# Performance work log

Hardware: AMD Instinct MI355X
Metric: run time of the kernel (lower is better)

Reference implementation:

```python
import jax, jax.numpy as jnp
import numpy as np
from jax.ops import segment_sum, segment_max

N_GENE, D_IN, HID, HEADS = 100000, 128, 128, 4
N_DRUG, N_DIS = 10000, 5000


def gcn_conv(x, src, dst, W, b, n):
    # PyG GCNConv: add self loops, symmetric deg^-1/2 normalization, scatter-add
    h = x @ W  # [n, hid]
    loop = jnp.arange(n)
    s = jnp.concatenate([src, loop])
    d = jnp.concatenate([dst, loop])
    deg = segment_sum(jnp.ones(d.shape[0], h.dtype), d, num_segments=n)
    dis = jnp.where(deg > 0, jax.lax.rsqrt(deg), 0.0)
    norm = dis[s] * dis[d]  # [E+n]
    return segment_sum(h[s] * norm[:, None], d, num_segments=n) + b


def gat_conv(xs, xd, src, dst, W, att_s, att_d, b, n_dst, heads=HEADS):
    # PyG GATConv (bipartite, shared lin, add_self_loops=False, concat=False)
    C = W.shape[1] // heads
    hs = (xs @ W).reshape(-1, heads, C)  # [Ns,H,C]
    hd = (xd @ W).reshape(-1, heads, C)  # [Nd,H,C]
    a_s = (hs * att_s).sum(-1)  # [Ns,H]
    a_d = (hd * att_d).sum(-1)  # [Nd,H]
    e = jax.nn.leaky_relu(a_s[src] + a_d[dst], 0.2)  # [E,H]
    m = segment_max(e, dst, num_segments=n_dst)
    m = jnp.where(jnp.isfinite(m), m, 0.0)
    ex = jnp.exp(e - m[dst])
    denom = segment_sum(ex, dst, num_segments=n_dst)
    alpha = ex / (denom[dst] + 1e-16)  # per-dst softmax
    out = segment_sum(hs[src] * alpha[:, :, None], dst, num_segments=n_dst)  # [Nd,H,C]
    return out.mean(axis=1) + b


def setup_inputs() -> dict:
    key = jax.random.key(0)
    ks = jax.random.split(key, 24)
    Eg, Ed, Ec = 1000000, 250000, 250000
    sc = 1.0 / np.sqrt(HID)
    inp = {
        'gene_nodes': jax.random.normal(ks[0], (N_GENE, D_IN), jnp.float32),
        'drug_edges': jnp.stack([jax.random.randint(ks[1], (Ed,), 0, N_DRUG),
                                 jax.random.randint(ks[2], (Ed,), 0, N_GENE)]),
        'disease_edges': jnp.stack([jax.random.randint(ks[3], (Ec,), 0, N_DIS),
                                    jax.random.randint(ks[4], (Ec,), 0, N_GENE)]),
        'gene_edges': jax.random.randint(ks[5], (2, Eg), 0, N_GENE),
        'gcn1_w': jax.random.normal(ks[6], (D_IN, HID), jnp.float32) * sc,
        'gcn1_b': jnp.zeros((HID,), jnp.float32),
        'gcn2_w': jax.random.normal(ks[7], (HID, HID), jnp.float32) * sc,
        'gcn2_b': jnp.zeros((HID,), jnp.float32),
        'drug_embed': jax.random.normal(ks[8], (N_DRUG, HID), jnp.float32),
        'disease_embed': jax.random.normal(ks[9], (N_DIS, HID), jnp.float32),
        'gat_d_w': jax.random.normal(ks[10], (HID, HEADS * HID), jnp.float32) * sc,
        'gat_d_att_src': jax.random.normal(ks[11], (HEADS, HID), jnp.float32) * sc,
        'gat_d_att_dst': jax.random.normal(ks[12], (HEADS, HID), jnp.float32) * sc,
        'gat_d_b': jnp.zeros((HID,), jnp.float32),
        'gat_c_w': jax.random.normal(ks[13], (HID, HEADS * HID), jnp.float32) * sc,
        'gat_c_att_src': jax.random.normal(ks[14], (HEADS, HID), jnp.float32) * sc,
        'gat_c_att_dst': jax.random.normal(ks[15], (HEADS, HID), jnp.float32) * sc,
        'gat_c_b': jnp.zeros((HID,), jnp.float32),
        'fuse_w': jax.random.normal(ks[16], (3 * HID, HID), jnp.float32) * sc,
        'fuse_b': jnp.zeros((HID,), jnp.float32),
    }
    return inp


def reference(gene_nodes, drug_edges, disease_edges, gene_edges,
              gcn1_w, gcn1_b, gcn2_w, gcn2_b, drug_embed, disease_embed,
              gat_d_w, gat_d_att_src, gat_d_att_dst, gat_d_b,
              gat_c_w, gat_c_att_src, gat_c_att_dst, gat_c_b,
              fuse_w, fuse_b):
    gs, gd = gene_edges[0], gene_edges[1]
    x = jax.nn.relu(gcn_conv(gene_nodes, gs, gd, gcn1_w, gcn1_b, N_GENE))
    x = jax.nn.relu(gcn_conv(x, gs, gd, gcn2_w, gcn2_b, N_GENE))
    # hetero GAT: drug->gene and disease->gene, HeteroConv aggr='mean'
    g_drug = gat_conv(drug_embed, x, drug_edges[0], drug_edges[1],
                      gat_d_w, gat_d_att_src, gat_d_att_dst, gat_d_b, N_GENE)
    g_dis = gat_conv(disease_embed, x, disease_edges[0], disease_edges[1],
                     gat_c_w, gat_c_att_src, gat_c_att_dst, gat_c_b, N_GENE)
    gene_out = 0.5 * (g_drug + g_dis)
    bg = gene_out.mean(axis=0, keepdims=True)   # [1,HID]
    bd = drug_embed.mean(axis=0, keepdims=True)
    bc = disease_embed.mean(axis=0, keepdims=True)
    return jnp.concatenate([bg, bd, bc], axis=-1) @ fuse_w + fuse_b  # [1,HID]
```

## Files before the change

kernel.cpp:

```cpp
#include <hip/hip_runtime.h>
#include <hip/hip_fp16.h>

#define NG 100000
#define NDR 10000
#define NDI 5000
#define NDOM (3 * NG + NDR + NDI)
#define NBUCK 616
#define BCHUNK 4096
#define EPT 16

typedef _Float16 f16x8 __attribute__((ext_vector_type(8)));
typedef float f32x4 __attribute__((ext_vector_type(4)));

__device__ __forceinline__ void atomAddF(float* p, float v) { unsafeAtomicAdd(p, v); }

static inline int cdiv_h(int a, int b) { return (a + b - 1) / b; }

__device__ __host__ __forceinline__ int bcap(int b) {
  return b < 586 ? 8192 : (b < 606 ? 24576 : 32768);
}
__device__ __host__ __forceinline__ int bbase(int b) {
  if (b < 586) return b * 8192;
  if (b < 606) return 586 * 8192 + (b - 586) * 24576;
  return 586 * 8192 + 20 * 24576 + (b - 606) * 32768;
}
#define NPAIR (586 * 8192 + 20 * 24576 + 10 * 32768)

__global__ __launch_bounds__(256) void k_front(const float* __restrict__ W1,
                                               const float* __restrict__ W2,
                                               const float* __restrict__ Wd,
                                               const float* __restrict__ Wc,
                                               const float* __restrict__ attd_d,
                                               const float* __restrict__ attd_c,
                                               __half* __restrict__ Wt1,
                                               __half* __restrict__ Wt2,
                                               __half* __restrict__ Wtd,
                                               __half* __restrict__ Wtc,
                                               float* __restrict__ watt,
                                               int* __restrict__ cursor616,
                                               const float* __restrict__ xd,
                                               float* __restrict__ od,
                                               const float* __restrict__ xc,
                                               float* __restrict__ oc) {
  int blk = blockIdx.x;
  int t = threadIdx.x;
  if (blk < 40) {
    __shared__ float tile[64][65];
    const float* W;
    __half* Wt;
    int N, k0, n0;
    if (blk < 4) { W = W1; Wt = Wt1; N = 128; k0 = (blk >> 1) * 64; n0 = (blk & 1) * 64; }
    else if (blk < 8) { int b = blk - 4; W = W2; Wt = Wt2; N = 128; k0 = (b >> 1) * 64; n0 = (b & 1) * 64; }
    else if (blk < 24) { int b = blk - 8; W = Wd; Wt = Wtd; N = 512; k0 = (b >> 3) * 64; n0 = (b & 7) * 64; }
    else { int b = blk - 24; W = Wc; Wt = Wtc; N = 512; k0 = (b >> 3) * 64; n0 = (b & 7) * 64; }
    for (int i = t; i < 4096; i += 256) {
      int r = i >> 6, c = i & 63;
      tile[r][c] = W[(size_t)(k0 + r) * N + n0 + c];
    }
    __syncthreads();
    for (int i = t; i < 4096; i += 256) {
      int k = i & 63, n = i >> 6;
      Wt[(size_t)(n0 + n) * 128 + k0 + k] = __float2half(tile[k][n]);
    }
    return;
  }
  if (blk < 44) {
    int slot = (blk - 40) * 256 + t;
    int i = slot >> 3, s8 = slot & 7;
    const float* W = (s8 < 4) ? Wd : Wc;
    const float* A = (s8 < 4) ? attd_d : attd_c;
    int h = s8 & 3;
    float s = 0.f;
    for (int cc = 0; cc < 128; cc++) s += W[(size_t)i * 512 + h * 128 + cc] * A[h * 128 + cc];
    watt[i * 8 + s8] = s;
    return;
  }
  if (blk == 44) {
    for (int i = t; i < NBUCK; i += 256) cursor616[i] = bbase(i);
    return;
  }
  int cb = blk - 45;
  int q = cb >= 79;
  const float* x = q ? xc : xd;
  float* o = q ? oc : od;
  int N = q ? NDI : NDR;
  int r0 = (q ? cb - 79 : cb) * 128 + (t >> 7) * 64;
  int col = t & 127;
  int r1 = min(r0 + 64, N);
  float acc = 0.f;
  for (int r = r0; r < r1; r++) acc += x[(size_t)r * 128 + col];
  if (r0 < N) atomAddF(&o[col], acc);
}

__device__ __forceinline__ void decode(int idx, const int* __restrict__ ge, int Eg_,
                                       const int* __restrict__ de, int Ed_,
                                       const int* __restrict__ ce, int Ec_,
                                       unsigned& node, unsigned& val) {
  int B1 = Eg_, B2 = Eg_ + Ed_, B3 = Eg_ + 2 * Ed_, B4 = B3 + Ec_;
  if (idx < B1) { node = (unsigned)ge[Eg_ + idx]; val = (unsigned)ge[idx]; }
  else if (idx < B2) { int i = idx - B1; node = NG + (unsigned)de[Ed_ + i]; val = (unsigned)de[i]; }
  else if (idx < B3) { int i = idx - B2; node = 3 * NG + (unsigned)de[i]; val = (unsigned)de[Ed_ + i]; }
  else if (idx < B4) { int i = idx - B3; node = 2 * NG + (unsigned)ce[Ec_ + i]; val = (unsigned)ce[i]; }
  else { int i = idx - B4; node = 3 * NG + NDR + (unsigned)ce[i]; val = (unsigned)ce[Ec_ + i]; }
}

__global__ __launch_bounds__(256) void k_binH(const int* __restrict__ ge, int Eg_,
                                              const int* __restrict__ de, int Ed_,
                                              const int* __restrict__ ce, int Ec_,
                                              int* __restrict__ cursor616,
                                              unsigned* __restrict__ pairs) {
  __shared__ int hist[NBUCK];
  int t = threadIdx.x;
  for (int i = t; i < NBUCK; i += 256) hist[i] = 0;
  __syncthreads();
  const int ME = Eg_ + 2 * (Ed_ + Ec_);
  int base = blockIdx.x * BCHUNK;
  int cnt = min(BCHUNK, ME - base);

  unsigned nodeR[EPT], valR[EPT];
#pragma unroll
  for (int k = 0; k < EPT; k++) {
    int j = t + k * 256;
    nodeR[k] = 0xFFFFFFFFu;
    if (j < cnt) decode(base + j, ge, Eg_, de, Ed_, ce, Ec_, nodeR[k], valR[k]);
  }
#pragma unroll
  for (int k = 0; k < EPT; k++)
    if (nodeR[k] != 0xFFFFFFFFu) atomicAdd(&hist[nodeR[k] >> 9], 1);
  __syncthreads();
  for (int b = t; b < NBUCK; b += 256) {
    int h = hist[b];
    hist[b] = h ? atomicAdd(&cursor616[b], h) : 0;
  }
  __syncthreads();
#pragma unroll
  for (int k = 0; k < EPT; k++) {
    if (nodeR[k] == 0xFFFFFFFFu) continue;
    unsigned b = nodeR[k] >> 9;
    int p = atomicAdd(&hist[b], 1);
    if (p < bbase(b) + bcap(b))
      pairs[p] = ((nodeR[k] - (b << 9)) << 17) | valR[k];
  }
}

__global__ __launch_bounds__(256) void k_scan616(const int* __restrict__ cursor616,
                                                 int* __restrict__ bucketbase) {
  __shared__ int s[256];
  int t = threadIdx.x;
  int loc[3];
  int sum = 0;
#pragma unroll
  for (int k = 0; k < 3; k++) {
    int b = 3 * t + k;
    int v = (b < NBUCK) ? min(cursor616[b] - bbase(b), bcap(b)) : 0;
    loc[k] = sum;
    sum += v;
  }
  s[t] = sum;
  __syncthreads();
  for (int off = 1; off < 256; off <<= 1) {
    int add = (t >= off) ? s[t - off] : 0;
    __syncthreads();
    s[t] += add;
    __syncthreads();
  }
  int excl = s[t] - sum;
#pragma unroll
  for (int k = 0; k < 3; k++) {
    int b = 3 * t + k;
    if (b < NBUCK) bucketbase[b] = excl + loc[k];
  }
}

__global__ __launch_bounds__(256) void k_placeAll(const int* __restrict__ cursor616,
                                                  const int* __restrict__ bucketbase,
                                                  const unsigned* __restrict__ pairs,
                                                  int* __restrict__ rowptr,
                                                  float* __restrict__ dis,
                                                  int* __restrict__ adj) {
  __shared__ int hist[512];
  __shared__ int scan[256];
  int b = blockIdx.x;
  int n0 = b << 9;
  int n1 = min(n0 + 512, NDOM);
  int t = threadIdx.x;
  hist[t] = 0;
  hist[t + 256] = 0;
  __syncthreads();
  int base = bbase(b);
  int cnt = min(cursor616[b] - base, bcap(b));
  for (int i = base + t; i < base + cnt; i += 256) atomicAdd(&hist[pairs[i] >> 17], 1);
  __syncthreads();
  int h0 = hist[2 * t], h1 = hist[2 * t + 1];
  int sum = h0 + h1;
  scan[t] = sum;
  __syncthreads();
  for (int off = 1; off < 256; off <<= 1) {
    int add = (t >= off) ? scan[t - off] : 0;
    __syncthreads();
    scan[t] += add;
    __syncthreads();
  }
  int excl = scan[t] - sum;
  int bb = bucketbase[b];
  int i0 = 2 * t, i1 = 2 * t + 1;
  int r0 = bb + excl, r1 = bb + excl + h0;
  if (n0 + i0 < n1) {
    rowptr[n0 + i0] = r0;
    if (n0 + i0 < NG) dis[n0 + i0] = rsqrtf((float)h0 + 1.0f);
  }
  if (n0 + i1 < n1) {
    rowptr[n0 + i1] = r1;
    if (n0 + i1 < NG) dis[n0 + i1] = rsqrtf((float)h1 + 1.0f);
    if (n0 + i1 == NDOM - 1) rowptr[NDOM] = r1 + h1;
  }
  if (n0 + i0 == NDOM - 1) rowptr[NDOM] = r0 + h0;
  __syncthreads();
  hist[i0] = r0;
  hist[i1] = r1;
  __syncthreads();
  for (int i = base + t; i < base + cnt; i += 256) {
    unsigned pr = pairs[i];
    int p = atomicAdd(&hist[pr >> 17], 1);
    adj[p] = (int)(pr & 0x1FFFFu);
  }
}

template <int INF16>
__device__ __forceinline__ void mgemm_body(char* lds, int bx, const void* __restrict__ Xv,
                                           const __half* __restrict__ Wt, int M,
                                           const float* __restrict__ dis,
                                           __half* __restrict__ hh) {
  char* As = lds;
  char* Bs = lds + 16 * 1024;
  const int t = threadIdx.x;
  const int row0 = bx * 64;

#pragma unroll
  for (int rep = 0; rep < 8; rep++) {
    int q = t + rep * 256;
    int r = q >> 4, c16 = (q & 15) * 16;
    uint4 v = *(const uint4*)((const char*)Wt + r * 256 + c16);
    *(uint4*)(Bs + ((r * 256 + c16) ^ ((r & 7) << 4))) = v;
  }
  if (INF16 == 0) {
    const float* X = (const float*)Xv;
#pragma unroll
    for (int rep = 0; rep < 8; rep++) {
      int q = t + rep * 256;
      int r = q >> 5, c4 = (q & 31) * 4;
      int gr = row0 + r;
      float4 xv = make_float4(0.f, 0.f, 0.f, 0.f);
      if (gr < M) xv = *(const float4*)&X[(size_t)gr * 128 + c4];
      __half2 h0 = __floats2half2_rn(xv.x, xv.y);
      __half2 h1 = __floats2half2_rn(xv.z, xv.w);
      uint2 pk;
      pk.x = *(unsigned*)&h0;
      pk.y = *(unsigned*)&h1;
      *(uint2*)(As + ((r * 256 + c4 * 2) ^ ((r & 7) << 4))) = pk;
    }
  } else {
    const __half* X = (const __half*)Xv;
#pragma unroll
    for (int rep = 0; rep < 4; rep++) {
      int q = t + rep * 256;
      int r = q >> 4, c16 = (q & 15) * 16;
      int gr = row0 + r;
      uint4 v = make_uint4(0u, 0u, 0u, 0u);
      if (gr < M) v = *(const uint4*)((const char*)X + (size_t)gr * 256 + c16);
      *(uint4*)(As + ((r * 256 + c16) ^ ((r & 7) << 4))) = v;
    }
  }
  __syncthreads();

  const int w = t >> 6, l = t & 63;
  const int lr = l & 15, lk = l >> 4;
  f32x4 acc[8] = {};
#pragma unroll
  for (int s = 0; s < 4; s++) {
    int arow = w * 16 + lr;
    f16x8 a = *(const f16x8*)(As + ((arow * 256 + lk * 16 + s * 64) ^ ((arow & 7) << 4)));
#pragma unroll
    for (int nt = 0; nt < 8; nt++) {
      int brow = nt * 16 + lr;
      f16x8 b = *(const f16x8*)(Bs + ((brow * 256 + lk * 16 + s * 64) ^ ((brow & 7) << 4)));
      acc[nt] = __builtin_amdgcn_mfma_f32_16x16x32_f16(a, b, acc[nt], 0, 0, 0);
    }
  }
  float ddv[4];
  int rowb = row0 + w * 16 + lk * 4;
#pragma unroll
  for (int j = 0; j < 4; j++) ddv[j] = (rowb + j < M) ? dis[rowb + j] : 0.f;
#pragma unroll
  for (int nt = 0; nt < 8; nt++) {
#pragma unroll
    for (int j = 0; j < 4; j++) {
      int row = rowb + j;
      if (row < M) hh[(size_t)row * 128 + nt * 16 + lr] = __float2half(acc[nt][j] * ddv[j]);
    }
  }
}

__device__ __forceinline__ void mgat_body(char* lds, int bxx, int h,
                                          const float* __restrict__ Xd,
                                          const float* __restrict__ Xc,
                                          const __half* __restrict__ Wtd,
                                          const __half* __restrict__ Wtc,
                                          const float* __restrict__ attSd,
                                          const float* __restrict__ attSc,
                                          __half* __restrict__ hsd,
                                          __half* __restrict__ hsc,
                                          float* __restrict__ a_s_d,
                                          float* __restrict__ a_s_c) {
  char* As = lds;
  char* Bs = lds + 16 * 1024;
  const int t = threadIdx.x;
  const int nbd = (NDR + 63) >> 6;
  const int q = bxx >= nbd;
  const int bx = q ? bxx - nbd : bxx;
  const int M = q ? NDI : NDR;
  const float* X = q ? Xc : Xd;
  const __half* Wt = q ? Wtc : Wtd;
  const float* attS = q ? attSc : attSd;
  __half* hs = q ? hsc : hsd;
  float* a_s = q ? a_s_c : a_s_d;
  const int row0 = bx * 64;
  const __half* Wth = Wt + (size_t)h * 128 * 128;

#pragma unroll
  for (int rep = 0; rep < 8; rep++) {
    int r = (t + rep * 256) >> 4, c16 = ((t + rep * 256) & 15) * 16;
    uint4 v = *(const uint4*)((const char*)Wth + r * 256 + c16);
    *(uint4*)(Bs + ((r * 256 + c16) ^ ((r & 7) << 4))) = v;
  }
#pragma unroll
  for (int rep = 0; rep < 8; rep++) {
    int qq = t + rep * 256;
    int r = qq >> 5, c4 = (qq & 31) * 4;
    int gr = row0 + r;
    float4 xv = make_float4(0.f, 0.f, 0.f, 0.f);
    if (gr < M) xv = *(const float4*)&X[(size_t)gr * 128 + c4];
    __half2 h0 = __floats2half2_rn(xv.x, xv.y);
    __half2 h1 = __floats2half2_rn(xv.z, xv.w);
    uint2 pk;
    pk.x = *(unsigned*)&h0;
    pk.y = *(unsigned*)&h1;
    *(uint2*)(As + ((r * 256 + c4 * 2) ^ ((r & 7) << 4))) = pk;
  }
  __syncthreads();

  const int w = t >> 6, l = t & 63;
  const int lr = l & 15, lk = l >> 4;
  f32x4 acc[8] = {};
#pragma unroll
  for (int s = 0; s < 4; s++) {
    int arow = w * 16 + lr;
    f16x8 a = *(const f16x8*)(As + ((arow * 256 + lk * 16 + s * 64) ^ ((arow & 7) << 4)));
#pragma unroll
    for (int nt = 0; nt < 8; nt++) {
      int brow = nt * 16 + lr;
      f16x8 b = *(const f16x8*)(Bs + ((brow * 256 + lk * 16 + s * 64) ^ ((brow & 7) << 4)));
      acc[nt] = __builtin_amdgcn_mfma_f32_16x16x32_f16(a, b, acc[nt], 0, 0, 0);
    }
  }
  float av[8];
#pragma unroll
  for (int nt = 0; nt < 8; nt++) av[nt] = attS[h * 128 + nt * 16 + lr];

  int rowb = row0 + w * 16 + lk * 4;
  float p[4] = {0.f, 0.f, 0.f, 0.f};
#pragma unroll
  for (int nt = 0; nt < 8; nt++) {
#pragma unroll
    for (int j = 0; j < 4; j++) {
      int row = rowb + j;
      if (row < M) hs[(size_t)row * 512 + h * 128 + nt * 16 + lr] = __float2half(acc[nt][j]);
      p[j] += acc[nt][j] * av[nt];
    }
  }
#pragma unroll
  for (int m = 1; m < 16; m <<= 1) {
#pragma unroll
    for (int j = 0; j < 4; j++) p[j] += __shfl_xor(p[j], m);
  }
  if (lr == 0) {
#pragma unroll
    for (int j = 0; j < 4; j++) {
      int row = rowb + j;
      if (row < M) a_s[(size_t)row * 4 + h] = p[j];
    }
  }
}

__global__ __launch_bounds__(256) void k_mm1(const float* __restrict__ X1,
                                             const __half* __restrict__ Wt1,
                                             const float* __restrict__ dis,
                                             __half* __restrict__ hh,
                                             const float* __restrict__ Xd,
                                             const float* __restrict__ Xc,
                                             const __half* __restrict__ Wtd,
                                             const __half* __restrict__ Wtc,
                                             const float* __restrict__ attSd,
                                             const float* __restrict__ attSc,
                                             __half* __restrict__ hsd,
                                             __half* __restrict__ hsc,
                                             float* __restrict__ a_s_d,
                                             float* __restrict__ a_s_c) {
  __shared__ __align__(16) char lds[48 * 1024];
  const int NB1 = (NG + 63) >> 6;
  if ((int)blockIdx.x < NB1) {
    mgemm_body<0>(lds, blockIdx.x, X1, Wt1, NG, dis, hh);
    return;
  }
  int r = blockIdx.x - NB1;
  mgat_body(lds, r >> 2, r & 3, Xd, Xc, Wtd, Wtc, attSd, attSc, hsd, hsc, a_s_d, a_s_c);
}

template <int INF16>
__global__ __launch_bounds__(256) void k_mgemm(const void* __restrict__ Xv,
                                               const __half* __restrict__ Wt, int M,
                                               const float* __restrict__ dis,
                                               __half* __restrict__ hh) {
  __shared__ __align__(16) char lds[48 * 1024];
  mgemm_body<INF16>(lds, blockIdx.x, Xv, Wt, M, dis, hh);
}

template <int FIN>
__global__ __launch_bounds__(256) void k_gather(const __half* __restrict__ hh,
                                                const int* __restrict__ rowptr,
                                                const int* __restrict__ adj,
                                                const float* __restrict__ dis,
                                                const float* __restrict__ b,
                                                const float* __restrict__ watt,
                                                void* __restrict__ outv, int n) {
  int wid = threadIdx.x >> 6;
  int lane = threadIdx.x & 63;
  int d = blockIdx.x * 4 + wid;
  if (d >= n) return;
  int p0 = rowptr[d], p1 = rowptr[d + 1];
  int c = lane * 2;
  float2 s;
  {
    unsigned v = *(const unsigned*)&hh[(size_t)d * 128 + c];
    s = __half22float2(*(__half2*)&v);
  }
  for (int base = p0; base < p1; base += 64) {
    int remain = p1 - base;
    int m = remain < 64 ? remain : 64;
    int idx = (lane < m) ? adj[base + lane] : 0;
    int j = 0;
    for (; j + 8 <= m; j += 8) {
      int nb[8];
      unsigned v[8];
#pragma unroll
      for (int u = 0; u < 8; u++) nb[u] = __shfl(idx, j + u);
#pragma unroll
      for (int u = 0; u < 8; u++) v[u] = *(const unsigned*)&hh[(size_t)nb[u] * 128 + c];
#pragma unroll
      for (int u = 0; u < 8; u++) {
        float2 f = __half22float2(*(__half2*)&v[u]);
        s.x += f.x;
        s.y += f.y;
      }
    }
    for (; j + 4 <= m; j += 4) {
      int nb[4];
      unsigned v[4];
#pragma unroll
      for (int u = 0; u < 4; u++) nb[u] = __shfl(idx, j + u);
#pragma unroll
      for (int u = 0; u < 4; u++) v[u] = *(const unsigned*)&hh[(size_t)nb[u] * 128 + c];
#pragma unroll
      for (int u = 0; u < 4; u++) {
        float2 f = __half22float2(*(__half2*)&v[u]);
        s.x += f.x;
        s.y += f.y;
      }
    }
    for (; j < m; j++) {
      int nb = __shfl(idx, j);
      unsigned v = *(const unsigned*)&hh[(size_t)nb * 128 + c];
      float2 f = __half22float2(*(__half2*)&v);
      s.x += f.x;
      s.y += f.y;
    }
  }
  float dd = dis[d];
  float x0 = fmaxf(dd * s.x + b[c], 0.f);
  float x1v = fmaxf(dd * s.y + b[c + 1], 0.f);
  if (FIN == 1) {
    __half* o = (__half*)outv;
    __half2 hv = __floats2half2_rn(x0, x1v);
    *(__half2*)&o[(size_t)d * 128 + c] = hv;
  } else {
    float* o = (float*)outv;
    float p[8];
    const float* w0 = &watt[c * 8];
#pragma unroll
    for (int h = 0; h < 8; h++) p[h] = x0 * w0[h] + x1v * w0[8 + h];
#pragma unroll
    for (int mm = 32; mm; mm >>= 1) {
#pragma unroll
      for (int h = 0; h < 8; h++) p[h] += __shfl_xor(p[h], mm);
    }
    if (lane == 0) {
      *(float4*)&o[(size_t)d * 8] = make_float4(p[0], p[1], p[2], p[3]);
      *(float4*)&o[(size_t)d * 8 + 4] = make_float4(p[4], p[5], p[6], p[7]);
    }
  }
}

__global__ __launch_bounds__(256) void k_edgeA(const int* __restrict__ rowptr,
                                               const int* __restrict__ adj,
                                               const float* __restrict__ a_s_d,
                                               const float* __restrict__ a_s_c,
                                               const float* __restrict__ att,
                                               float* __restrict__ denom_d,
                                               float* __restrict__ denom_c) {
  int nb1 = (NG + 255) >> 8;
  int blk = blockIdx.x;
  int q = blk >= nb1;
  int d = (blk - (q ? nb1 : 0)) * 256 + threadIdx.x;
  if (d >= NG) return;
  const int* rp = rowptr + NG + (q ? NG : 0);
  const float* a_s = q ? a_s_c : a_s_d;
  float* den = q ? denom_c : denom_d;
  int p0 = rp[d], p1 = rp[d + 1];
  float4 ad4 = *(const float4*)&att[(size_t)d * 8 + q * 4];
  float4 acc = make_float4(0.f, 0.f, 0.f, 0.f);
  for (int p = p0; p < p1; p++) {
    int s = adj[p];
    float4 as4 = *(const float4*)&a_s[(size_t)s * 4];
    float v0 = as4.x + ad4.x, v1 = as4.y + ad4.y, v2 = as4.z + ad4.z, v3 = as4.w + ad4.w;
    v0 = v0 > 0.f ? v0 : 0.2f * v0;
    v1 = v1 > 0.f ? v1 : 0.2f * v1;
    v2 = v2 > 0.f ? v2 : 0.2f * v2;
    v3 = v3 > 0.f ? v3 : 0.2f * v3;
    acc.x += __expf(fminf(v0, 50.f));
    acc.y += __expf(fminf(v1, 50.f));
    acc.z += __expf(fminf(v2, 50.f));
    acc.w += __expf(fminf(v3, 50.f));
  }
  *(float4*)&den[(size_t)d * 4] = acc;
}

__global__ __launch_bounds__(256) void k_edgeB(const int* __restrict__ rowptr,
                                               const int* __restrict__ adj,
                                               const float* __restrict__ a_s_d,
                                               const float* __restrict__ a_s_c,
                                               const float* __restrict__ att,
                                               const float* __restrict__ denom_d,
                                               const float* __restrict__ denom_c,
                                               float* __restrict__ wsrc_d,
                                               float* __restrict__ wsrc_c) {
  int gw = (blockIdx.x * 256 + threadIdx.x) >> 6;
  int lane = threadIdx.x & 63;
  int q = gw >= NDR;
  int s = q ? gw - NDR : gw;
  if (q && s >= NDI) return;
  const int* rp = rowptr + 3 * NG + (q ? NDR : 0);
  const float* a_s = q ? a_s_c : a_s_d;
  const float* den = q ? denom_c : denom_d;
  float* ws = q ? wsrc_c : wsrc_d;
  int p0 = rp[s], p1 = rp[s + 1];
  float4 as4 = *(const float4*)&a_s[(size_t)s * 4];
  int attoff = q * 4;
  float4 acc = make_float4(0.f, 0.f, 0.f, 0.f);
  for (int p = p0 + lane; p < p1; p += 64) {
    int d = adj[p];
    float4 ad4 = *(const float4*)&att[(size_t)d * 8 + attoff];
    float4 dn = *(const float4*)&den[(size_t)d * 4];
    float v0 = as4.x + ad4.x, v1 = as4.y + ad4.y, v2 = as4.z + ad4.z, v3 = as4.w + ad4.w;
    v0 = v0 > 0.f ? v0 : 0.2f * v0;
    v1 = v1 > 0.f ? v1 : 0.2f * v1;
    v2 = v2 > 0.f ? v2 : 0.2f * v2;
    v3 = v3 > 0.f ? v3 : 0.2f * v3;
    acc.x += __expf(fminf(v0, 50.f)) / (dn.x + 1e-16f);
    acc.y += __expf(fminf(v1, 50.f)) / (dn.y + 1e-16f);
    acc.z += __expf(fminf(v2, 50.f)) / (dn.z + 1e-16f);
    acc.w += __expf(fminf(v3, 50.f)) / (dn.w + 1e-16f);
  }
#pragma unroll
  for (int m = 1; m < 64; m <<= 1) {
    acc.x += __shfl_xor(acc.x, m);
    acc.y += __shfl_xor(acc.y, m);
    acc.z += __shfl_xor(acc.z, m);
    acc.w += __shfl_xor(acc.w, m);
  }
  if (lane == 0) *(float4*)&ws[(size_t)s * 4] = acc;
}

__global__ __launch_bounds__(512) void k_sum(const __half* __restrict__ hs_d,
                                             const float* __restrict__ wsrc_d,
                                             float* __restrict__ S_d,
                                             const __half* __restrict__ hs_c,
                                             const float* __restrict__ wsrc_c,
                                             float* __restrict__ S_c) {
  int t = threadIdx.x;
  const int nws_d = (NDR + 63) >> 6;
  int blk = blockIdx.x;
  int q = blk >= nws_d;
  const __half* hs = q ? hs_c : hs_d;
  const float* wsrc = q ? wsrc_c : wsrc_d;
  float* S = q ? S_c : S_d;
  int N = q ? NDI : NDR;
  int r0 = (q ? blk - nws_d : blk) * 64;
  int h = t >> 7;
  int r1 = min(r0 + 64, N);
  float acc = 0.f;
  for (int r = r0; r < r1; r++) acc += wsrc[r * 4 + h] * __half2float(hs[(size_t)r * 512 + t]);
  atomAddF(&S[t], acc);
}

__global__ __launch_bounds__(128) void k_final(const float* __restrict__ S_d,
                                               const float* __restrict__ S_c,
                                               const float* __restrict__ bdsum,
                                               const float* __restrict__ bcsum,
                                               const float* __restrict__ bd_bias,
                                               const float* __restrict__ bc_bias,
                                               const float* __restrict__ fuse_w,
                                               const float* __restrict__ fuse_b,
                                               float* __restrict__ out) {
  __shared__ float cat[384];
  int t = threadIdx.x;
  float sd = S_d[t] + S_d[128 + t] + S_d[256 + t] + S_d[384 + t];
  float sc = S_c[t] + S_c[128 + t] + S_c[256 + t] + S_c[384 + t];
  const float inv = 1.0f / (4.0f * (float)NG);
  cat[t] = 0.5f * (sd * inv + bd_bias[t] + sc * inv + bc_bias[t]);
  cat[128 + t] = bdsum[t] * (1.0f / (float)NDR);
  cat[256 + t] = bcsum[t] * (1.0f / (float)NDI);
  __syncthreads();
  float o = fuse_b[t];
  for (int k = 0; k < 384; k++) o += cat[k] * fuse_w[k * 128 + t];
  out[t] = o;
}

extern "C" void kernel_launch(void* const* d_in, const int* in_sizes, int n_in,
                              void* d_out, int out_size, void* d_ws, size_t ws_size,
                              hipStream_t stream) {
  const float* gene_nodes   = (const float*)d_in[0];
  const int*   drug_edges   = (const int*)d_in[1];
  const int*   dise_edges   = (const int*)d_in[2];
  const int*   gene_edges   = (const int*)d_in[3];
  const float* gcn1_w       = (const float*)d_in[4];
  const float* gcn1_b       = (const float*)d_in[5];
  const float* gcn2_w       = (const float*)d_in[6];
  const float* gcn2_b       = (const float*)d_in[7];
  const float* drug_embed   = (const float*)d_in[8];
  const float* dise_embed   = (const float*)d_in[9];
  const float* gat_d_w      = (const float*)d_in[10];
  const float* gat_d_att_s  = (const float*)d_in[11];
  const float* gat_d_att_d  = (const float*)d_in[12];
  const float* gat_d_b      = (const float*)d_in[13];
  const float* gat_c_w      = (const float*)d_in[14];
  const float* gat_c_att_s  = (const float*)d_in[15];
  const float* gat_c_att_d  = (const float*)d_in[16];
  const float* gat_c_b      = (const float*)d_in[17];
  const float* fuse_w       = (const float*)d_in[18];
  const float* fuse_b       = (const float*)d_in[19];
  const int Ed = in_sizes[1] / 2;
  const int Ec = in_sizes[2] / 2;
  const int Eg = in_sizes[3] / 2;
  float* out = (float*)d_out;
  (void)n_in; (void)out_size; (void)ws_size;

  const int ME = Eg + 2 * (Ed + Ec);

  char* w = (char*)d_ws;
  auto alloc = [&](size_t n) {
    char* p = w;
    w += (n + 511) & ~(size_t)511;
    return p;
  };
  char* z0 = w;
  float* S_d        = (float*)alloc(512 * 4);
  float* S_c        = (float*)alloc(512 * 4);
  float* bdsum      = (float*)alloc(512);
  float* bcsum      = (float*)alloc(512);
  size_t zbytes = (size_t)(w - z0);
  float* denom_d    = (float*)alloc((size_t)NG * 16);
  float* denom_c    = (float*)alloc((size_t)NG * 16);
  float* wsrc_d     = (float*)alloc((size_t)NDR * 16);
  float* wsrc_c     = (float*)alloc((size_t)NDI * 16);
  float* dis        = (float*)alloc((size_t)NG * 4);
  float* watt       = (float*)alloc(128 * 8 * 4);
  float* att        = (float*)alloc((size_t)NG * 8 * 4);
  float* a_s_d      = (float*)alloc((size_t)NDR * 16);
  float* a_s_c      = (float*)alloc((size_t)NDI * 16);
  int* rowptr       = (int*)alloc((size_t)(NDOM + 1) * 4);
  int* cursor616    = (int*)alloc((size_t)NBUCK * 4);
  int* bucketbase   = (int*)alloc((size_t)(NBUCK + 1) * 4);
  int* adj          = (int*)alloc((size_t)ME * 4);
  unsigned* pairs   = (unsigned*)alloc((size_t)NPAIR * 4);
  __half* Wt1       = (__half*)alloc((size_t)128 * 128 * 2);
  __half* Wt2       = (__half*)alloc((size_t)128 * 128 * 2);
  __half* Wtd       = (__half*)alloc((size_t)512 * 128 * 2);
  __half* Wtc       = (__half*)alloc((size_t)512 * 128 * 2);
  __half* hh        = (__half*)alloc((size_t)NG * 128 * 2);
  __half* x1        = (__half*)alloc((size_t)NG * 128 * 2);
  __half* hs_d      = (__half*)alloc((size_t)NDR * 512 * 2);
  __half* hs_c      = (__half*)alloc((size_t)NDI * 512 * 2);

  hipMemsetAsync(z0, 0, zbytes, stream);

  k_front<<<164, 256, 0, stream>>>(gcn1_w, gcn2_w, gat_d_w, gat_c_w, gat_d_att_d, gat_c_att_d,
                                   Wt1, Wt2, Wtd, Wtc, watt, cursor616,
                                   drug_embed, bdsum, dise_embed, bcsum);

  k_binH<<<cdiv_h(ME, BCHUNK), 256, 0, stream>>>(gene_edges, Eg, drug_edges, Ed, dise_edges, Ec,
                                                 cursor616, pairs);
  k_scan616<<<1, 256, 0, stream>>>(cursor616, bucketbase);
  k_placeAll<<<NBUCK, 256, 0, stream>>>(cursor616, bucketbase, pairs, rowptr, dis, adj);

  int nb1 = cdiv_h(NG, 64);
  int nbg = (cdiv_h(NDR, 64) + cdiv_h(NDI, 64)) * 4;
  k_mm1<<<nb1 + nbg, 256, 0, stream>>>(gene_nodes, Wt1, dis, hh,
                                       drug_embed, dise_embed, Wtd, Wtc,
                                       gat_d_att_s, gat_c_att_s, hs_d, hs_c, a_s_d, a_s_c);

  k_gather<1><<<cdiv_h(NG, 4), 256, 0, stream>>>(hh, rowptr, adj, dis, gcn1_b, nullptr, x1, NG);

  k_mgemm<1><<<nb1, 256, 0, stream>>>(x1, Wt2, NG, dis, hh);
  k_gather<2><<<cdiv_h(NG, 4), 256, 0, stream>>>(hh, rowptr, adj, dis, gcn2_b, watt, att, NG);

  k_edgeA<<<2 * cdiv_h(NG, 256), 256, 0, stream>>>(rowptr, adj, a_s_d, a_s_c, att, denom_d, denom_c);
  k_edgeB<<<cdiv_h((NDR + NDI) * 64, 256), 256, 0, stream>>>(rowptr, adj, a_s_d, a_s_c, att,
                                                             denom_d, denom_c, wsrc_d, wsrc_c);

  k_sum<<<cdiv_h(NDR, 64) + cdiv_h(NDI, 64), 512, 0, stream>>>(hs_d, wsrc_d, S_d,
                                                               hs_c, wsrc_c, S_c);

  k_final<<<1, 128, 0, stream>>>(S_d, S_c, bdsum, bcsum, gat_d_b, gat_c_b, fuse_w, fuse_b, out);
}
```

Baseline: 328.3 us.

## Store GCN features in FP8 and merge edge binning into front kernel

The per-node GCN intermediate features written by the GEMMs and read by the neighbor gather are now stored as FP8 instead of FP16. This halves the bytes moved in the random-access gather over a million edges. Separately, the edge-binning pass is merged into the weight-transpose/front kernel, with zero-initialized counts replacing the precomputed cursor, which removes one launch and one dependency. FP8 storage adds quantization error to the GCN activations and may break accuracy tolerance.

```diff
diff --git a/kernel.cpp b/kernel.cpp
--- a/kernel.cpp
+++ b/kernel.cpp
@@ -11,8 +11,17 @@
 
 typedef _Float16 f16x8 __attribute__((ext_vector_type(8)));
 typedef float f32x4 __attribute__((ext_vector_type(4)));
+typedef float f32x2 __attribute__((ext_vector_type(2)));
 
 __device__ __forceinline__ void atomAddF(float* p, float v) { unsafeAtomicAdd(p, v); }
+
+__device__ __forceinline__ float2 fp8x2_f32(unsigned short v) {
+  f32x2 r = __builtin_amdgcn_cvt_pk_f32_fp8((int)v, false);
+  return make_float2(r[0], r[1]);
+}
+__device__ __forceinline__ unsigned char f32_fp8(float v) {
+  return (unsigned char)(__builtin_amdgcn_cvt_pk_fp8_f32(v, v, 0, false) & 0xFF);
+}
 
 static inline int cdiv_h(int a, int b) { return (a + b - 1) / b; }
 
@@ -26,7 +35,24 @@
 }
 #define NPAIR (586 * 8192 + 20 * 24576 + 10 * 32768)
 
-__global__ __launch_bounds__(256) void k_front(const float* __restrict__ W1,
+__device__ __forceinline__ void decode(int idx, const int* __restrict__ ge, int Eg_,
+                                       const int* __restrict__ de, int Ed_,
+                                       const int* __restrict__ ce, int Ec_,
+                                       unsigned& node, unsigned& val) {
+  int B1 = Eg_, B2 = Eg_ + Ed_, B3 = Eg_ + 2 * Ed_, B4 = B3 + Ec_;
+  if (idx < B1) { node = (unsigned)ge[Eg_ + idx]; val = (unsigned)ge[idx]; }
+  else if (idx < B2) { int i = idx - B1; node = NG + (unsigned)de[Ed_ + i]; val = (unsigned)de[i]; }
+  else if (idx < B3) { int i = idx - B2; node = 3 * NG + (unsigned)de[i]; val = (unsigned)de[Ed_ + i]; }
+  else if (idx < B4) { int i = idx - B3; node = 2 * NG + (unsigned)ce[Ec_ + i]; val = (unsigned)ce[i]; }
+  else { int i = idx - B4; node = 3 * NG + NDR + (unsigned)ce[i]; val = (unsigned)ce[Ec_ + i]; }
+}
+
+__global__ __launch_bounds__(256) void k_build(const int* __restrict__ ge, int Eg_,
+                                               const int* __restrict__ de, int Ed_,
+                                               const int* __restrict__ ce, int Ec_,
+                                               int* __restrict__ count616,
+                                               unsigned* __restrict__ pairs,
+                                               const float* __restrict__ W1,
                                                const float* __restrict__ W2,
                                                const float* __restrict__ Wd,
                                                const float* __restrict__ Wc,
@@ -37,22 +63,56 @@
                                                __half* __restrict__ Wtd,
                                                __half* __restrict__ Wtc,
                                                float* __restrict__ watt,
-                                               int* __restrict__ cursor616,
                                                const float* __restrict__ xd,
                                                float* __restrict__ od,
                                                const float* __restrict__ xc,
                                                float* __restrict__ oc) {
+  const int ME = Eg_ + 2 * (Ed_ + Ec_);
+  const int NBB = (ME + BCHUNK - 1) / BCHUNK;
   int blk = blockIdx.x;
   int t = threadIdx.x;
-  if (blk < 40) {
+  if (blk < NBB) {
+    __shared__ int hist[NBUCK];
+    for (int i = t; i < NBUCK; i += 256) hist[i] = 0;
+    __syncthreads();
+    int base = blk * BCHUNK;
+    int cnt = min(BCHUNK, ME - base);
+    unsigned nodeR[EPT], valR[EPT];
+#pragma unroll
+    for (int k = 0; k < EPT; k++) {
+      int j = t + k * 256;
+      nodeR[k] = 0xFFFFFFFFu;
+      if (j < cnt) decode(base + j, ge, Eg_, de, Ed_, ce, Ec_, nodeR[k], valR[k]);
+    }
+#pragma unroll
+    for (int k = 0; k < EPT; k++)
+      if (nodeR[k] != 0xFFFFFFFFu) atomicAdd(&hist[nodeR[k] >> 9], 1);
+    __syncthreads();
+    for (int b = t; b < NBUCK; b += 256) {
+      int h = hist[b];
+      hist[b] = h ? (bbase(b) + atomicAdd(&count616[b], h)) : 0;
+    }
+    __syncthreads();
+#pragma unroll
+    for (int k = 0; k < EPT; k++) {
+      if (nodeR[k] == 0xFFFFFFFFu) continue;
+      unsigned b = nodeR[k] >> 9;
+      int p = atomicAdd(&hist[b], 1);
+      if (p < bbase(b) + bcap(b))
+        pairs[p] = ((nodeR[k] - (b << 9)) << 17) | valR[k];
+    }
+    return;
+  }
+  int fb = blk - NBB;
+  if (fb < 40) {
     __shared__ float tile[64][65];
     const float* W;
     __half* Wt;
     int N, k0, n0;
-    if (blk < 4) { W = W1; Wt = Wt1; N = 128; k0 = (blk >> 1) * 64; n0 = (blk & 1) * 64; }
-    else if (blk < 8) { int b = blk - 4; W = W2; Wt = Wt2; N = 128; k0 = (b >> 1) * 64; n0 = (b & 1) * 64; }
-    else if (blk < 24) { int b = blk - 8; W = Wd; Wt = Wtd; N = 512; k0 = (b >> 3) * 64; n0 = (b & 7) * 64; }
-    else { int b = blk - 24; W = Wc; Wt = Wtc; N = 512; k0 = (b >> 3) * 64; n0 = (b & 7) * 64; }
+    if (fb < 4) { W = W1; Wt = Wt1; N = 128; k0 = (fb >> 1) * 64; n0 = (fb & 1) * 64; }
+    else if (fb < 8) { int b = fb - 4; W = W2; Wt = Wt2; N = 128; k0 = (b >> 1) * 64; n0 = (b & 1) * 64; }
+    else if (fb < 24) { int b = fb - 8; W = Wd; Wt = Wtd; N = 512; k0 = (b >> 3) * 64; n0 = (b & 7) * 64; }
+    else { int b = fb - 24; W = Wc; Wt = Wtc; N = 512; k0 = (b >> 3) * 64; n0 = (b & 7) * 64; }
     for (int i = t; i < 4096; i += 256) {
       int r = i >> 6, c = i & 63;
       tile[r][c] = W[(size_t)(k0 + r) * N + n0 + c];
@@ -64,8 +124,8 @@
     }
     return;
   }
-  if (blk < 44) {
-    int slot = (blk - 40) * 256 + t;
+  if (fb < 44) {
+    int slot = (fb - 40) * 256 + t;
     int i = slot >> 3, s8 = slot & 7;
     const float* W = (s8 < 4) ? Wd : Wc;
     const float* A = (s8 < 4) ? attd_d : attd_c;
@@ -75,11 +135,7 @@
     watt[i * 8 + s8] = s;
     return;
   }
-  if (blk == 44) {
-    for (int i = t; i < NBUCK; i += 256) cursor616[i] = bbase(i);
-    return;
-  }
-  int cb = blk - 45;
+  int cb = fb - 44;
   int q = cb >= 79;
   const float* x = q ? xc : xd;
   float* o = q ? oc : od;
@@ -92,58 +148,7 @@
   if (r0 < N) atomAddF(&o[col], acc);
 }
 
-__device__ __forceinline__ void decode(int idx, const int* __restrict__ ge, int Eg_,
-                                       const int* __restrict__ de, int Ed_,
-                                       const int* __restrict__ ce, int Ec_,
-                                       unsigned& node, unsigned& val) {
-  int B1 = Eg_, B2 = Eg_ + Ed_, B3 = Eg_ + 2 * Ed_, B4 = B3 + Ec_;
-  if (idx < B1) { node = (unsigned)ge[Eg_ + idx]; val = (unsigned)ge[idx]; }
-  else if (idx < B2) { int i = idx - B1; node = NG + (unsigned)de[Ed_ + i]; val = (unsigned)de[i]; }
-  else if (idx < B3) { int i = idx - B2; node = 3 * NG + (unsigned)de[i]; val = (unsigned)de[Ed_ + i]; }
-  else if (idx < B4) { int i = idx - B3; node = 2 * NG + (unsigned)ce[Ec_ + i]; val = (unsigned)ce[i]; }
-  else { int i = idx - B4; node = 3 * NG + NDR + (unsigned)ce[i]; val = (unsigned)ce[Ec_ + i]; }
-}
-
-__global__ __launch_bounds__(256) void k_binH(const int* __restrict__ ge, int Eg_,
-                                              const int* __restrict__ de, int Ed_,
-                                              const int* __restrict__ ce, int Ec_,
-                                              int* __restrict__ cursor616,
-                                              unsigned* __restrict__ pairs) {
-  __shared__ int hist[NBUCK];
-  int t = threadIdx.x;
-  for (int i = t; i < NBUCK; i += 256) hist[i] = 0;
-  __syncthreads();
-  const int ME = Eg_ + 2 * (Ed_ + Ec_);
-  int base = blockIdx.x * BCHUNK;
-  int cnt = min(BCHUNK, ME - base);
-
-  unsigned nodeR[EPT], valR[EPT];
-#pragma unroll
-  for (int k = 0; k < EPT; k++) {
-    int j = t + k * 256;
-    nodeR[k] = 0xFFFFFFFFu;
-    if (j < cnt) decode(base + j, ge, Eg_, de, Ed_, ce, Ec_, nodeR[k], valR[k]);
-  }
-#pragma unroll
-  for (int k = 0; k < EPT; k++)
-    if (nodeR[k] != 0xFFFFFFFFu) atomicAdd(&hist[nodeR[k] >> 9], 1);
-  __syncthreads();
-  for (int b = t; b < NBUCK; b += 256) {
-    int h = hist[b];
-    hist[b] = h ? atomicAdd(&cursor616[b], h) : 0;
-  }
-  __syncthreads();
-#pragma unroll
-  for (int k = 0; k < EPT; k++) {
-    if (nodeR[k] == 0xFFFFFFFFu) continue;
-    unsigned b = nodeR[k] >> 9;
-    int p = atomicAdd(&hist[b], 1);
-    if (p < bbase(b) + bcap(b))
-      pairs[p] = ((nodeR[k] - (b << 9)) << 17) | valR[k];
-  }
-}
-
-__global__ __launch_bounds__(256) void k_scan616(const int* __restrict__ cursor616,
+__global__ __launch_bounds__(256) void k_scan616(const int* __restrict__ count616,
                                                  int* __restrict__ bucketbase) {
   __shared__ int s[256];
   int t = threadIdx.x;
@@ -152,7 +157,7 @@
 #pragma unroll
   for (int k = 0; k < 3; k++) {
     int b = 3 * t + k;
-    int v = (b < NBUCK) ? min(cursor616[b] - bbase(b), bcap(b)) : 0;
+    int v = (b < NBUCK) ? min(count616[b], bcap(b)) : 0;
     loc[k] = sum;
     sum += v;
   }
@@ -172,7 +177,7 @@
   }
 }
 
-__global__ __launch_bounds__(256) void k_placeAll(const int* __restrict__ cursor616,
+__global__ __launch_bounds__(256) void k_placeAll(const int* __restrict__ count616,
                                                   const int* __restrict__ bucketbase,
                                                   const unsigned* __restrict__ pairs,
                                                   int* __restrict__ rowptr,
@@ -188,7 +193,7 @@
   hist[t + 256] = 0;
   __syncthreads();
   int base = bbase(b);
-  int cnt = min(cursor616[b] - base, bcap(b));
+  int cnt = min(count616[b], bcap(b));
   for (int i = base + t; i < base + cnt; i += 256) atomicAdd(&hist[pairs[i] >> 17], 1);
   __syncthreads();
   int h0 = hist[2 * t], h1 = hist[2 * t + 1];
@@ -230,7 +235,7 @@
 __device__ __forceinline__ void mgemm_body(char* lds, int bx, const void* __restrict__ Xv,
                                            const __half* __restrict__ Wt, int M,
                                            const float* __restrict__ dis,
-                                           __half* __restrict__ hh) {
+                                           unsigned char* __restrict__ hh) {
   char* As = lds;
   char* Bs = lds + 16 * 1024;
   const int t = threadIdx.x;
@@ -296,7 +301,7 @@
 #pragma unroll
     for (int j = 0; j < 4; j++) {
       int row = rowb + j;
-      if (row < M) hh[(size_t)row * 128 + nt * 16 + lr] = __float2half(acc[nt][j] * ddv[j]);
+      if (row < M) hh[(size_t)row * 128 + nt * 16 + lr] = f32_fp8(acc[nt][j] * ddv[j]);
     }
   }
 }
@@ -395,7 +400,7 @@
 __global__ __launch_bounds__(256) void k_mm1(const float* __restrict__ X1,
                                              const __half* __restrict__ Wt1,
                                              const float* __restrict__ dis,
-                                             __half* __restrict__ hh,
+                                             unsigned char* __restrict__ hh,
                                              const float* __restrict__ Xd,
                                              const float* __restrict__ Xc,
                                              const __half* __restrict__ Wtd,
@@ -420,13 +425,13 @@
 __global__ __launch_bounds__(256) void k_mgemm(const void* __restrict__ Xv,
                                                const __half* __restrict__ Wt, int M,
                                                const float* __restrict__ dis,
-                                               __half* __restrict__ hh) {
+                                               unsigned char* __restrict__ hh) {
   __shared__ __align__(16) char lds[48 * 1024];
   mgemm_body<INF16>(lds, blockIdx.x, Xv, Wt, M, dis, hh);
 }
 
 template <int FIN>
-__global__ __launch_bounds__(256) void k_gather(const __half* __restrict__ hh,
+__global__ __launch_bounds__(256) void k_gather(const unsigned char* __restrict__ hh,
                                                 const int* __restrict__ rowptr,
                                                 const int* __restrict__ adj,
                                                 const float* __restrict__ dis,
@@ -441,8 +446,8 @@
   int c = lane * 2;
   float2 s;
   {
-    unsigned v = *(const unsigned*)&hh[(size_t)d * 128 + c];
-    s = __half22float2(*(__half2*)&v);
+    unsigned short v = *(const unsigned short*)&hh[(size_t)d * 128 + c];
+    s = fp8x2_f32(v);
   }
   for (int base = p0; base < p1; base += 64) {
     int remain = p1 - base;
@@ -451,36 +456,36 @@
     int j = 0;
     for (; j + 8 <= m; j += 8) {
       int nb[8];
-      unsigned v[8];
+      unsigned short v[8];
 #pragma unroll
       for (int u = 0; u < 8; u++) nb[u] = __shfl(idx, j + u);
 #pragma unroll
-      for (int u = 0; u < 8; u++) v[u] = *(const unsigned*)&hh[(size_t)nb[u] * 128 + c];
+      for (int u = 0; u < 8; u++) v[u] = *(const unsigned short*)&hh[(size_t)nb[u] * 128 + c];
 #pragma unroll
       for (int u = 0; u < 8; u++) {
-        float2 f = __half22float2(*(__half2*)&v[u]);
+        float2 f = fp8x2_f32(v[u]);
         s.x += f.x;
         s.y += f.y;
       }
     }
     for (; j + 4 <= m; j += 4) {
       int nb[4];
-      unsigned v[4];
+      unsigned short v[4];
 #pragma unroll
       for (int u = 0; u < 4; u++) nb[u] = __shfl(idx, j + u);
 #pragma unroll
-      for (int u = 0; u < 4; u++) v[u] = *(const unsigned*)&hh[(size_t)nb[u] * 128 + c];
+      for (int u = 0; u < 4; u++) v[u] = *(const unsigned short*)&hh[(size_t)nb[u] * 128 + c];
 #pragma unroll
       for (int u = 0; u < 4; u++) {
-        float2 f = __half22float2(*(__half2*)&v[u]);
+        float2 f = fp8x2_f32(v[u]);
         s.x += f.x;
         s.y += f.y;
       }
     }
     for (; j < m; j++) {
       int nb = __shfl(idx, j);
-      unsigned v = *(const unsigned*)&hh[(size_t)nb * 128 + c];
-      float2 f = __half22float2(*(__half2*)&v);
+      unsigned short v = *(const unsigned short*)&hh[(size_t)nb * 128 + c];
+      float2 f = fp8x2_f32(v);
       s.x += f.x;
       s.y += f.y;
     }
@@ -665,6 +670,7 @@
   (void)n_in; (void)out_size; (void)ws_size;
 
   const int ME = Eg + 2 * (Ed + Ec);
+  const int NBB = cdiv_h(ME, BCHUNK);
 
   char* w = (char*)d_ws;
   auto alloc = [&](size_t n) {
@@ -677,6 +683,7 @@
   float* S_c        = (float*)alloc(512 * 4);
   float* bdsum      = (float*)alloc(512);
   float* bcsum      = (float*)alloc(512);
+  int* count616     = (int*)alloc((size_t)NBUCK * 4);
   size_t zbytes = (size_t)(w - z0);
   float* denom_d    = (float*)alloc((size_t)NG * 16);
   float* denom_c    = (float*)alloc((size_t)NG * 16);
@@ -688,7 +695,6 @@
   float* a_s_d      = (float*)alloc((size_t)NDR * 16);
   float* a_s_c      = (float*)alloc((size_t)NDI * 16);
   int* rowptr       = (int*)alloc((size_t)(NDOM + 1) * 4);
-  int* cursor616    = (int*)alloc((size_t)NBUCK * 4);
   int* bucketbase   = (int*)alloc((size_t)(NBUCK + 1) * 4);
   int* adj          = (int*)alloc((size_t)ME * 4);
   unsigned* pairs   = (unsigned*)alloc((size_t)NPAIR * 4);
@@ -696,21 +702,20 @@
   __half* Wt2       = (__half*)alloc((size_t)128 * 128 * 2);
   __half* Wtd       = (__half*)alloc((size_t)512 * 128 * 2);
   __half* Wtc       = (__half*)alloc((size_t)512 * 128 * 2);
-  __half* hh        = (__half*)alloc((size_t)NG * 128 * 2);
+  unsigned char* hh = (unsigned char*)alloc((size_t)NG * 128);
   __half* x1        = (__half*)alloc((size_t)NG * 128 * 2);
   __half* hs_d      = (__half*)alloc((size_t)NDR * 512 * 2);
   __half* hs_c      = (__half*)alloc((size_t)NDI * 512 * 2);
 
   hipMemsetAsync(z0, 0, zbytes, stream);
 
-  k_front<<<164, 256, 0, stream>>>(gcn1_w, gcn2_w, gat_d_w, gat_c_w, gat_d_att_d, gat_c_att_d,
-                                   Wt1, Wt2, Wtd, Wtc, watt, cursor616,
-                                   drug_embed, bdsum, dise_embed, bcsum);
-
-  k_binH<<<cdiv_h(ME, BCHUNK), 256, 0, stream>>>(gene_edges, Eg, drug_edges, Ed, dise_edges, Ec,
-                                                 cursor616, pairs);
-  k_scan616<<<1, 256, 0, stream>>>(cursor616, bucketbase);
-  k_placeAll<<<NBUCK, 256, 0, stream>>>(cursor616, bucketbase, pairs, rowptr, dis, adj);
+  k_build<<<NBB + 163, 256, 0, stream>>>(gene_edges, Eg, drug_edges, Ed, dise_edges, Ec,
+                                         count616, pairs,
+                                         gcn1_w, gcn2_w, gat_d_w, gat_c_w, gat_d_att_d, gat_c_att_d,
+                                         Wt1, Wt2, Wtd, Wtc, watt,
+                                         drug_embed, bdsum, dise_embed, bcsum);
+  k_scan616<<<1, 256, 0, stream>>>(count616, bucketbase);
+  k_placeAll<<<NBUCK, 256, 0, stream>>>(count616, bucketbase, pairs, rowptr, dis, adj);
 
   int nb1 = cdiv_h(NG, 64);
   int nbg = (cdiv_h(NDR, 64) + cdiv_h(NDI, 64)) * 4;
```

After: 305.5 us, median of 2. -6.9%, faster.
